# Kernel optimization log

Hardware: AMD Instinct MI355X
Metric: run time of the kernel (lower is better)

## Reference

```python
import jax, jax.numpy as jnp
import numpy as np

DIM = 256


def setup_inputs() -> dict:
    key = jax.random.key(0)
    ks = jax.random.split(key, 10)
    d = DIM
    inp = {
        "agent": jax.random.normal(ks[0], (64, d), dtype=jnp.float32),
        "x": jax.random.normal(ks[1], (8, 4096, d), dtype=jnp.float32),
        # parameters (stored as [in, out]; y = x @ W + b)
        "W_qkv": jax.random.normal(ks[2], (d, 3 * d), dtype=jnp.float32) * (d ** -0.5),
        "b_qkv": jnp.zeros((3 * d,), dtype=jnp.float32),
        "W_agent": jax.random.normal(ks[3], (d, 2 * d), dtype=jnp.float32) * (d ** -0.5),
        "b_agent": jnp.zeros((2 * d,), dtype=jnp.float32),
        "W_fc1": jax.random.normal(ks[4], (d, d), dtype=jnp.float32) * (d ** -0.5),
        "b_fc1": jnp.zeros((d,), dtype=jnp.float32),
        "W_fc2": jax.random.normal(ks[5], (d, d), dtype=jnp.float32) * (d ** -0.5),
        "b_fc2": jnp.zeros((d,), dtype=jnp.float32),
    }
    return inp


def reference(agent, x, W_qkv, b_qkv, W_agent, b_agent, W_fc1, b_fc1, W_fc2, b_fc2):
    d = x.shape[-1]
    scale = d ** -0.5
    # qkv projection of tokens: [B,N,3d] -> q,k,v each [B,N,d]
    qkv = x @ W_qkv + b_qkv
    q, k, v = jnp.split(qkv, 3, axis=-1)
    # agent projection: [K,2d] -> q_agent,k_agent each [K,d]
    ag = agent @ W_agent + b_agent
    q_agent, k_agent = jnp.split(ag, 2, axis=-1)
    # stage 1: agents attend over tokens -> [B,K,N]
    attn1 = jax.nn.softmax(jnp.einsum('kd,bnd->bkn', q_agent, k) * scale, axis=-1)
    va = jnp.einsum('bkn,bnd->bkd', attn1, v)  # [B,K,d]
    va = va @ W_fc1 + b_fc1
    # stage 2: tokens attend over agents -> [B,N,K]
    attn2 = jax.nn.softmax(jnp.einsum('bnd,kd->bnk', q, k_agent) * scale, axis=-1)
    out = jnp.einsum('bnk,bkd->bnd', attn2, va)  # [B,N,d]
    out = out @ W_fc2 + b_fc2
    return out + x
```

## Files before the change

kernel.cpp:

```cpp
#include <hip/hip_runtime.h>
#include <stdint.h>
#include <string.h>

#define BB 8
#define NN 4096
#define DD 256
#define SCALE 0.0625f
#define XS2 264

using frag_ab = __attribute__((ext_vector_type(8))) short;
using frag_cd = __attribute__((ext_vector_type(4))) float;

__device__ __forceinline__ unsigned short f2bf(float f) {
    union { float f; unsigned u; } a; a.f = f;
    unsigned r = a.u + 0x7FFFu + ((a.u >> 16) & 1u);
    return (unsigned short)(r >> 16);
}
__device__ __forceinline__ float bf2f(unsigned short h) {
    union { unsigned u; float f; } a; a.u = ((unsigned)h) << 16;
    return a.f;
}

__global__ __launch_bounds__(256) void k_setup(
    const float* __restrict__ agent, const float* __restrict__ Wag,
    const float* __restrict__ bag, const float* __restrict__ Wqkv,
    const float* __restrict__ bqkv, const float* __restrict__ Wfc1,
    const float* __restrict__ bfc1, const float* __restrict__ Wfc2,
    unsigned short* __restrict__ P12t, float* __restrict__ c2,
    unsigned short* __restrict__ W3b, float* __restrict__ b3)
{
    __shared__ float arow[256];
    __shared__ float red[256];
    const int bx = blockIdx.x, tid = threadIdx.x;
    if (bx < 128) {
        const int c = bx;
        const int woff = (c < 64) ? 256 : 0;
        const int aoff = (c < 64) ? 0 : 256;
        const int row = c & 63;
        float s = bag[aoff + tid];
        for (int o = 0; o < 256; ++o) s += agent[row * 256 + o] * Wag[o * 512 + aoff + tid];
        arow[tid] = s;
        __syncthreads();
        float p = 0.f;
        for (int o = 0; o < 256; ++o) p += Wqkv[tid * 768 + woff + o] * arow[o];
        P12t[(size_t)c * 256 + tid] = f2bf(SCALE * p);
        if (c >= 64) {
            red[tid] = bqkv[woff + tid] * arow[tid];
            __syncthreads();
            for (int st = 128; st; st >>= 1) {
                if (tid < st) red[tid] += red[tid + st];
                __syncthreads();
            }
            if (tid == 0) c2[c - 64] = SCALE * red[0];
        }
    } else if (bx < 384) {
        const int i = bx - 128;
        float t = 0.f;
        for (int o = 0; o < 256; ++o) t += Wqkv[i * 768 + 512 + o] * Wfc1[o * 256 + tid];
        arow[tid] = t;
        __syncthreads();
        float p = 0.f;
        for (int k = 0; k < 256; ++k) p += arow[k] * Wfc2[k * 256 + tid];
        W3b[(size_t)i * 256 + tid] = f2bf(p);
    } else {
        float t = bfc1[tid];
        for (int o = 0; o < 256; ++o) t += bqkv[512 + o] * Wfc1[o * 256 + tid];
        arow[tid] = t;
        __syncthreads();
        float p = 0.f;
        for (int k = 0; k < 256; ++k) p += arow[k] * Wfc2[k * 256 + tid];
        b3[tid] = p;
    }
}

__global__ __launch_bounds__(256) void k_xlogits(
    const float* __restrict__ x, const unsigned short* __restrict__ P12t,
    const float* __restrict__ c2, unsigned short* __restrict__ xt,
    unsigned short* __restrict__ p1, unsigned short* __restrict__ p2b,
    float* __restrict__ statS)
{
    __shared__ unsigned short xtile[32 * XS2];
    __shared__ unsigned short Bs[128 * 72];
    __shared__ float Ss[2][64];
    const int chunk = blockIdx.x, b = blockIdx.y;
    const int n0 = chunk * 32;
    const int tid = threadIdx.x;
    const int w = tid >> 6, lane = tid & 63;
    const int ml = lane & 15, q = lane >> 4;
    const int rt = w & 1, cg = w >> 1;

#pragma unroll
    for (int p = 0; p < 8; ++p) {
        int idx = p * 256 + tid;
        int tok = idx >> 6, d = (idx & 63) * 4;
        float4 v = *(const float4*)&x[(size_t)(b * 4096 + n0 + tok) * 256 + d];
        unsigned short u[4] = {f2bf(v.x), f2bf(v.y), f2bf(v.z), f2bf(v.w)};
        uint2 pk; memcpy(&pk, u, 8);
        *(uint2*)&xtile[tok * XS2 + d] = pk;
    }
    __syncthreads();
#pragma unroll
    for (int p = 0; p < 8; ++p) {
        int idx = p * 256 + tid;
        int d = idx >> 3, seg = idx & 7;
        unsigned short u[4];
#pragma unroll
        for (int k = 0; k < 4; ++k) u[k] = xtile[(seg * 4 + k) * XS2 + d];
        uint2 pk; memcpy(&pk, u, 8);
        *(uint2*)&xt[(size_t)(b * 256 + d) * 4096 + n0 + seg * 4] = pk;
    }

    frag_cd acc[4];
#pragma unroll
    for (int j = 0; j < 4; ++j)
#pragma unroll
        for (int r = 0; r < 4; ++r) acc[j][r] = 0.f;

    for (int kb = 0; kb < 256; kb += 64) {
        __syncthreads();
#pragma unroll
        for (int p = 0; p < 4; ++p) {
            int idx = p * 256 + tid;
            int r = idx >> 3, c = (idx & 7) * 8;
            *(uint4*)&Bs[r * 72 + c] = *(const uint4*)&P12t[(size_t)r * 256 + kb + c];
        }
        __syncthreads();
#pragma unroll
        for (int ks = 0; ks < 2; ++ks) {
            const int kk = ks * 32 + q * 8;
            frag_ab a = *(const frag_ab*)&xtile[(rt * 16 + ml) * XS2 + kb + kk];
#pragma unroll
            for (int j = 0; j < 4; ++j) {
                frag_ab bf = *(const frag_ab*)&Bs[(cg * 64 + j * 16 + ml) * 72 + kk];
                acc[j] = __builtin_amdgcn_mfma_f32_16x16x32_bf16(a, bf, acc[j], 0, 0, 0);
            }
        }
    }

    if (cg == 0) {
#pragma unroll
        for (int j = 0; j < 4; ++j) {
            const int ag = j * 16 + ml;
            float e[4];
#pragma unroll
            for (int r = 0; r < 4; ++r) e[r] = __expf(acc[j][r]);
            unsigned short u[4] = {f2bf(e[0]), f2bf(e[1]), f2bf(e[2]), f2bf(e[3])};
            uint2 pk; memcpy(&pk, u, 8);
            *(uint2*)&p1[(size_t)(b * 64 + ag) * 4096 + n0 + rt * 16 + q * 4] = pk;
            float s = e[0] + e[1] + e[2] + e[3];
            s += __shfl_xor(s, 16);
            s += __shfl_xor(s, 32);
            if (q == 0) Ss[rt][ag] = s;
        }
    } else {
        float cc[4];
#pragma unroll
        for (int j = 0; j < 4; ++j) cc[j] = c2[j * 16 + ml];
#pragma unroll
        for (int r = 0; r < 4; ++r) {
            float e[4], s = 0.f;
#pragma unroll
            for (int j = 0; j < 4; ++j) {
                e[j] = __expf(acc[j][r] + cc[j]);
                s += e[j];
            }
#pragma unroll
            for (int mask = 1; mask <= 8; mask <<= 1) s += __shfl_xor(s, mask);
            float inv = 1.f / s;
            const int tok = n0 + rt * 16 + q * 4 + r;
#pragma unroll
            for (int j = 0; j < 4; ++j)
                p2b[(size_t)(b * 4096 + tok) * 64 + j * 16 + ml] = f2bf(e[j] * inv);
        }
    }
    __syncthreads();
    if (tid < 64)
        statS[(size_t)(b * 64 + tid) * 128 + chunk] = Ss[0][tid] + Ss[1][tid];
}

__global__ __launch_bounds__(256) void k_va(
    const unsigned short* __restrict__ p1, const float* __restrict__ statS,
    const unsigned short* __restrict__ xt, unsigned short* __restrict__ part)
{
    __shared__ unsigned short As[64 * 152];
    __shared__ unsigned short Bs[64 * 152];
    __shared__ float Rs[4][64], Inv[64];
    const int s = blockIdx.x, dh = blockIdx.y, b = blockIdx.z;
    const int tid = threadIdx.x;
    const int w = tid >> 6, lane = tid & 63;
    const int ml = lane & 15, q = lane >> 4;

#pragma unroll
    for (int p = 0; p < 4; ++p) {
        int idx = p * 256 + tid;
        int r = idx >> 4, c = (idx & 15) * 8;
        *(uint4*)&Bs[r * 152 + c] =
            *(const uint4*)&xt[(size_t)(b * 256 + dh * 64 + r) * 4096 + s * 128 + c];
    }
    {
        const int a = tid & 63, qq = tid >> 6;
        const float* ps = &statS[(size_t)(b * 64 + a) * 128 + qq * 32];
        float sum = 0.f;
#pragma unroll
        for (int p = 0; p < 8; ++p) {
            float4 s4 = *(const float4*)&ps[p * 4];
            sum += s4.x + s4.y + s4.z + s4.w;
        }
        Rs[qq][a] = sum;
    }
    __syncthreads();
    if (tid < 64)
        Inv[tid] = 1.f / (Rs[0][tid] + Rs[1][tid] + Rs[2][tid] + Rs[3][tid]);
    __syncthreads();
#pragma unroll
    for (int p = 0; p < 8; ++p) {
        int idx4 = (p * 256 + tid) * 4;
        int ag = idx4 >> 7, t = idx4 & 127;
        uint2 pk = *(const uint2*)&p1[(size_t)(b * 64 + ag) * 4096 + s * 128 + t];
        unsigned short in[4]; memcpy(in, &pk, 8);
        float inv = Inv[ag];
        unsigned short u[4] = {f2bf(bf2f(in[0]) * inv), f2bf(bf2f(in[1]) * inv),
                               f2bf(bf2f(in[2]) * inv), f2bf(bf2f(in[3]) * inv)};
        uint2 po; memcpy(&po, u, 8);
        *(uint2*)&As[ag * 152 + t] = po;
    }
    __syncthreads();

    frag_cd acc[4];
#pragma unroll
    for (int i = 0; i < 4; ++i)
#pragma unroll
        for (int r = 0; r < 4; ++r) acc[i][r] = 0.f;
#pragma unroll
    for (int ks = 0; ks < 4; ++ks) {
        const int kk = ks * 32 + q * 8;
        frag_ab bf = *(const frag_ab*)&Bs[(w * 16 + ml) * 152 + kk];
#pragma unroll
        for (int i = 0; i < 4; ++i) {
            frag_ab a = *(const frag_ab*)&As[(i * 16 + ml) * 152 + kk];
            acc[i] = __builtin_amdgcn_mfma_f32_16x16x32_bf16(a, bf, acc[i], 0, 0, 0);
        }
    }
    const int d = dh * 64 + w * 16 + ml;
#pragma unroll
    for (int i = 0; i < 4; ++i)
#pragma unroll
        for (int r = 0; r < 4; ++r)
            part[(size_t)((s * 8 + b) * 64 + i * 16 + q * 4 + r) * 256 + d] =
                f2bf(acc[i][r]);
}

__global__ __launch_bounds__(256) void k_fc(
    const unsigned short* __restrict__ part, const unsigned short* __restrict__ W3b,
    const float* __restrict__ b3, unsigned short* __restrict__ va3t)
{
    __shared__ float rowb[256];
    const int row = blockIdx.x, tid = threadIdx.x;
    const int b = row >> 6, agc = row & 63;
    float sv = 0.f;
    for (int s = 0; s < 32; ++s)
        sv += bf2f(part[(size_t)((s * 8 + b) * 64 + agc) * 256 + tid]);
    rowb[tid] = sv;
    __syncthreads();
    float s2 = b3[tid];
    for (int k = 0; k < 256; ++k) s2 += rowb[k] * bf2f(W3b[(size_t)k * 256 + tid]);
    va3t[(size_t)(b * 256 + tid) * 64 + agc] = f2bf(s2);
}

__global__ __launch_bounds__(256) void k_stage2(
    const unsigned short* __restrict__ p2b, const unsigned short* __restrict__ va3t,
    const float* __restrict__ x, const float* __restrict__ bfc2,
    float* __restrict__ out)
{
    __shared__ unsigned short Vs[256 * 72];
    __shared__ unsigned short Ps[64 * 72];
    const int n0 = blockIdx.x * 64, b = blockIdx.y;
    const int tid = threadIdx.x;
    const int w = tid >> 6, lane = tid & 63;
    const int ml = lane & 15, q = lane >> 4;

#pragma unroll
    for (int p = 0; p < 8; ++p) {
        int idx = p * 256 + tid;
        int r = idx >> 3, c = (idx & 7) * 8;
        *(uint4*)&Vs[r * 72 + c] = *(const uint4*)&va3t[(size_t)(b * 256 + r) * 64 + c];
    }
#pragma unroll
    for (int p = 0; p < 2; ++p) {
        int idx = p * 256 + tid;
        int r = idx >> 3, c = (idx & 7) * 8;
        *(uint4*)&Ps[r * 72 + c] = *(const uint4*)&p2b[(size_t)(b * 4096 + n0 + r) * 64 + c];
    }
    __syncthreads();

    frag_cd acc[4][4];
#pragma unroll
    for (int i = 0; i < 4; ++i)
#pragma unroll
        for (int j = 0; j < 4; ++j)
#pragma unroll
            for (int r = 0; r < 4; ++r) acc[i][j][r] = 0.f;
#pragma unroll
    for (int ks = 0; ks < 2; ++ks) {
        const int kk = ks * 32 + q * 8;
        frag_ab a[4], bf[4];
#pragma unroll
        for (int i = 0; i < 4; ++i)
            a[i] = *(const frag_ab*)&Vs[(w * 64 + i * 16 + ml) * 72 + kk];
#pragma unroll
        for (int j = 0; j < 4; ++j)
            bf[j] = *(const frag_ab*)&Ps[(j * 16 + ml) * 72 + kk];
#pragma unroll
        for (int i = 0; i < 4; ++i)
#pragma unroll
            for (int j = 0; j < 4; ++j)
                acc[i][j] = __builtin_amdgcn_mfma_f32_16x16x32_bf16(
                    a[i], bf[j], acc[i][j], 0, 0, 0);
    }

#pragma unroll
    for (int i = 0; i < 4; ++i) {
        const int d0 = w * 64 + i * 16 + q * 4;
        float4 bias = *(const float4*)&bfc2[d0];
#pragma unroll
        for (int j = 0; j < 4; ++j) {
            const int tok = n0 + j * 16 + ml;
            size_t ad = (size_t)(b * 4096 + tok) * 256 + d0;
            float4 xr = *(const float4*)&x[ad];
            float4 o;
            o.x = acc[i][j][0] + bias.x + xr.x;
            o.y = acc[i][j][1] + bias.y + xr.y;
            o.z = acc[i][j][2] + bias.z + xr.z;
            o.w = acc[i][j][3] + bias.w + xr.w;
            *(float4*)&out[ad] = o;
        }
    }
}

extern "C" void kernel_launch(void* const* d_in, const int* in_sizes, int n_in,
                              void* d_out, int out_size, void* d_ws, size_t ws_size,
                              hipStream_t stream) {
    const float* agent = (const float*)d_in[0];
    const float* x     = (const float*)d_in[1];
    const float* Wqkv  = (const float*)d_in[2];
    const float* bqkv  = (const float*)d_in[3];
    const float* Wag   = (const float*)d_in[4];
    const float* bag   = (const float*)d_in[5];
    const float* Wfc1  = (const float*)d_in[6];
    const float* bfc1  = (const float*)d_in[7];
    const float* Wfc2  = (const float*)d_in[8];
    const float* bfc2  = (const float*)d_in[9];
    float* out = (float*)d_out;

    char* w = (char*)d_ws;
    size_t off = 0;
    unsigned short* xt   = (unsigned short*)(w + off); off += (size_t)BB * DD * NN * 2;
    unsigned short* p1   = (unsigned short*)(w + off); off += (size_t)BB * 64 * NN * 2;
    unsigned short* p2b  = (unsigned short*)(w + off); off += (size_t)BB * NN * 64 * 2;
    unsigned short* part = (unsigned short*)(w + off); off += (size_t)32 * BB * 64 * 256 * 2;
    float* statS = (float*)(w + off); off += (size_t)BB * 64 * 128 * 4;
    unsigned short* P12t = (unsigned short*)(w + off); off += (size_t)128 * 256 * 2;
    float* c2   = (float*)(w + off); off += 256 * 4;
    unsigned short* W3b = (unsigned short*)(w + off); off += (size_t)256 * 256 * 2;
    float* b3   = (float*)(w + off); off += 256 * 4;
    unsigned short* va3t = (unsigned short*)(w + off); off += (size_t)BB * DD * 64 * 2;

    k_setup<<<385, 256, 0, stream>>>(agent, Wag, bag, Wqkv, bqkv, Wfc1, bfc1, Wfc2,
                                     P12t, c2, W3b, b3);
    k_xlogits<<<dim3(128, BB), 256, 0, stream>>>(x, P12t, c2, xt, p1, p2b, statS);
    k_va<<<dim3(32, 4, BB), 256, 0, stream>>>(p1, statS, xt, part);
    k_fc<<<512, 256, 0, stream>>>(part, W3b, b3, va3t);
    k_stage2<<<dim3(64, BB), 256, 0, stream>>>(p2b, va3t, x, bfc2, out);
}
```

Baseline: 169.0 us.

## Load MFMA operands directly from global memory and shrink stage2 tiles

Several kernels stop staging operands in shared memory. k_xlogits reads the P12t fragments and k_va reads the xt fragments straight from global memory, which drops their LDS buffers and barriers. k_stage2 halves its token tile to 32, doubles its grid, prefetches the residual x early and loads fragments directly from global. k_setup vectorises its dot product with float4, and k_va widens its p1 loads to 16 bytes. Direct global fragment loads depend on L2 and L1 hits and may produce less coalesced accesses.

```diff
diff --git a/kernel.cpp b/kernel.cpp
--- a/kernel.cpp
+++ b/kernel.cpp
@@ -42,7 +42,13 @@
         arow[tid] = s;
         __syncthreads();
         float p = 0.f;
-        for (int o = 0; o < 256; ++o) p += Wqkv[tid * 768 + woff + o] * arow[o];
+        const float* wr = &Wqkv[tid * 768 + woff];
+#pragma unroll 8
+        for (int o4 = 0; o4 < 64; ++o4) {
+            float4 wv = *(const float4*)&wr[o4 * 4];
+            float4 av = *(const float4*)&arow[o4 * 4];
+            p += wv.x * av.x + wv.y * av.y + wv.z * av.z + wv.w * av.w;
+        }
         P12t[(size_t)c * 256 + tid] = f2bf(SCALE * p);
         if (c >= 64) {
             red[tid] = bqkv[woff + tid] * arow[tid];
@@ -80,7 +86,6 @@
     float* __restrict__ statS)
 {
     __shared__ unsigned short xtile[32 * XS2];
-    __shared__ unsigned short Bs[128 * 72];
     __shared__ float Ss[2][64];
     const int chunk = blockIdx.x, b = blockIdx.y;
     const int n0 = chunk * 32;
@@ -116,22 +121,15 @@
 #pragma unroll
         for (int r = 0; r < 4; ++r) acc[j][r] = 0.f;
 
-    for (int kb = 0; kb < 256; kb += 64) {
-        __syncthreads();
-#pragma unroll
-        for (int p = 0; p < 4; ++p) {
-            int idx = p * 256 + tid;
-            int r = idx >> 3, c = (idx & 7) * 8;
-            *(uint4*)&Bs[r * 72 + c] = *(const uint4*)&P12t[(size_t)r * 256 + kb + c];
-        }
-        __syncthreads();
+#pragma unroll
+    for (int kb = 0; kb < 4; ++kb) {
 #pragma unroll
         for (int ks = 0; ks < 2; ++ks) {
-            const int kk = ks * 32 + q * 8;
-            frag_ab a = *(const frag_ab*)&xtile[(rt * 16 + ml) * XS2 + kb + kk];
+            const int kk = kb * 64 + ks * 32 + q * 8;
+            frag_ab a = *(const frag_ab*)&xtile[(rt * 16 + ml) * XS2 + kk];
 #pragma unroll
             for (int j = 0; j < 4; ++j) {
-                frag_ab bf = *(const frag_ab*)&Bs[(cg * 64 + j * 16 + ml) * 72 + kk];
+                frag_ab bf = *(const frag_ab*)&P12t[(size_t)(cg * 64 + j * 16 + ml) * 256 + kk];
                 acc[j] = __builtin_amdgcn_mfma_f32_16x16x32_bf16(a, bf, acc[j], 0, 0, 0);
             }
         }
@@ -183,20 +181,12 @@
     const unsigned short* __restrict__ xt, unsigned short* __restrict__ part)
 {
     __shared__ unsigned short As[64 * 152];
-    __shared__ unsigned short Bs[64 * 152];
     __shared__ float Rs[4][64], Inv[64];
     const int s = blockIdx.x, dh = blockIdx.y, b = blockIdx.z;
     const int tid = threadIdx.x;
     const int w = tid >> 6, lane = tid & 63;
     const int ml = lane & 15, q = lane >> 4;
 
-#pragma unroll
-    for (int p = 0; p < 4; ++p) {
-        int idx = p * 256 + tid;
-        int r = idx >> 4, c = (idx & 15) * 8;
-        *(uint4*)&Bs[r * 152 + c] =
-            *(const uint4*)&xt[(size_t)(b * 256 + dh * 64 + r) * 4096 + s * 128 + c];
-    }
     {
         const int a = tid & 63, qq = tid >> 6;
         const float* ps = &statS[(size_t)(b * 64 + a) * 128 + qq * 32];
@@ -213,16 +203,17 @@
         Inv[tid] = 1.f / (Rs[0][tid] + Rs[1][tid] + Rs[2][tid] + Rs[3][tid]);
     __syncthreads();
 #pragma unroll
-    for (int p = 0; p < 8; ++p) {
-        int idx4 = (p * 256 + tid) * 4;
-        int ag = idx4 >> 7, t = idx4 & 127;
-        uint2 pk = *(const uint2*)&p1[(size_t)(b * 64 + ag) * 4096 + s * 128 + t];
-        unsigned short in[4]; memcpy(in, &pk, 8);
+    for (int p = 0; p < 4; ++p) {
+        int idx8 = (p * 256 + tid) * 8;
+        int ag = idx8 >> 7, t = idx8 & 127;
+        uint4 pk = *(const uint4*)&p1[(size_t)(b * 64 + ag) * 4096 + s * 128 + t];
+        unsigned short in[8]; memcpy(in, &pk, 16);
         float inv = Inv[ag];
-        unsigned short u[4] = {f2bf(bf2f(in[0]) * inv), f2bf(bf2f(in[1]) * inv),
-                               f2bf(bf2f(in[2]) * inv), f2bf(bf2f(in[3]) * inv)};
-        uint2 po; memcpy(&po, u, 8);
-        *(uint2*)&As[ag * 152 + t] = po;
+        unsigned short u[8];
+#pragma unroll
+        for (int k = 0; k < 8; ++k) u[k] = f2bf(bf2f(in[k]) * inv);
+        uint4 po; memcpy(&po, u, 16);
+        *(uint4*)&As[ag * 152 + t] = po;
     }
     __syncthreads();
 
@@ -234,7 +225,8 @@
 #pragma unroll
     for (int ks = 0; ks < 4; ++ks) {
         const int kk = ks * 32 + q * 8;
-        frag_ab bf = *(const frag_ab*)&Bs[(w * 16 + ml) * 152 + kk];
+        frag_ab bf = *(const frag_ab*)&xt[(size_t)(b * 256 + dh * 64 + w * 16 + ml) * 4096 +
+                                          s * 128 + kk];
 #pragma unroll
         for (int i = 0; i < 4; ++i) {
             frag_ab a = *(const frag_ab*)&As[(i * 16 + ml) * 152 + kk];
@@ -272,66 +264,59 @@
     const float* __restrict__ x, const float* __restrict__ bfc2,
     float* __restrict__ out)
 {
-    __shared__ unsigned short Vs[256 * 72];
-    __shared__ unsigned short Ps[64 * 72];
-    const int n0 = blockIdx.x * 64, b = blockIdx.y;
+    const int n0 = blockIdx.x * 32, b = blockIdx.y;
     const int tid = threadIdx.x;
     const int w = tid >> 6, lane = tid & 63;
     const int ml = lane & 15, q = lane >> 4;
 
-#pragma unroll
-    for (int p = 0; p < 8; ++p) {
-        int idx = p * 256 + tid;
-        int r = idx >> 3, c = (idx & 7) * 8;
-        *(uint4*)&Vs[r * 72 + c] = *(const uint4*)&va3t[(size_t)(b * 256 + r) * 64 + c];
-    }
-#pragma unroll
-    for (int p = 0; p < 2; ++p) {
-        int idx = p * 256 + tid;
-        int r = idx >> 3, c = (idx & 7) * 8;
-        *(uint4*)&Ps[r * 72 + c] = *(const uint4*)&p2b[(size_t)(b * 4096 + n0 + r) * 64 + c];
-    }
-    __syncthreads();
-
-    frag_cd acc[4][4];
+    float4 xr[4][2];
 #pragma unroll
     for (int i = 0; i < 4; ++i)
 #pragma unroll
-        for (int j = 0; j < 4; ++j)
-#pragma unroll
-            for (int r = 0; r < 4; ++r) acc[i][j][r] = 0.f;
+        for (int j = 0; j < 2; ++j)
+            xr[i][j] = *(const float4*)&x[(size_t)(b * 4096 + n0 + j * 16 + ml) * 256 +
+                                          w * 64 + i * 16 + q * 4];
+
+    frag_ab a[4][2], bf[2][2];
 #pragma unroll
     for (int ks = 0; ks < 2; ++ks) {
         const int kk = ks * 32 + q * 8;
-        frag_ab a[4], bf[4];
 #pragma unroll
         for (int i = 0; i < 4; ++i)
-            a[i] = *(const frag_ab*)&Vs[(w * 64 + i * 16 + ml) * 72 + kk];
-#pragma unroll
-        for (int j = 0; j < 4; ++j)
-            bf[j] = *(const frag_ab*)&Ps[(j * 16 + ml) * 72 + kk];
+            a[i][ks] = *(const frag_ab*)&va3t[(size_t)(b * 256 + w * 64 + i * 16 + ml) * 64 + kk];
+#pragma unroll
+        for (int j = 0; j < 2; ++j)
+            bf[j][ks] = *(const frag_ab*)&p2b[(size_t)(b * 4096 + n0 + j * 16 + ml) * 64 + kk];
+    }
+
+    frag_cd acc[4][2];
+#pragma unroll
+    for (int i = 0; i < 4; ++i)
+#pragma unroll
+        for (int j = 0; j < 2; ++j)
+#pragma unroll
+            for (int r = 0; r < 4; ++r) acc[i][j][r] = 0.f;
+#pragma unroll
+    for (int ks = 0; ks < 2; ++ks)
 #pragma unroll
         for (int i = 0; i < 4; ++i)
 #pragma unroll
-            for (int j = 0; j < 4; ++j)
+            for (int j = 0; j < 2; ++j)
                 acc[i][j] = __builtin_amdgcn_mfma_f32_16x16x32_bf16(
-                    a[i], bf[j], acc[i][j], 0, 0, 0);
-    }
+                    a[i][ks], bf[j][ks], acc[i][j], 0, 0, 0);
 
 #pragma unroll
     for (int i = 0; i < 4; ++i) {
         const int d0 = w * 64 + i * 16 + q * 4;
         float4 bias = *(const float4*)&bfc2[d0];
 #pragma unroll
-        for (int j = 0; j < 4; ++j) {
-            const int tok = n0 + j * 16 + ml;
-            size_t ad = (size_t)(b * 4096 + tok) * 256 + d0;
-            float4 xr = *(const float4*)&x[ad];
+        for (int j = 0; j < 2; ++j) {
+            size_t ad = (size_t)(b * 4096 + n0 + j * 16 + ml) * 256 + d0;
             float4 o;
-            o.x = acc[i][j][0] + bias.x + xr.x;
-            o.y = acc[i][j][1] + bias.y + xr.y;
-            o.z = acc[i][j][2] + bias.z + xr.z;
-            o.w = acc[i][j][3] + bias.w + xr.w;
+            o.x = acc[i][j][0] + bias.x + xr[i][j].x;
+            o.y = acc[i][j][1] + bias.y + xr[i][j].y;
+            o.z = acc[i][j][2] + bias.z + xr[i][j].z;
+            o.w = acc[i][j][3] + bias.w + xr[i][j].w;
             *(float4*)&out[ad] = o;
         }
     }
@@ -370,5 +355,5 @@
     k_xlogits<<<dim3(128, BB), 256, 0, stream>>>(x, P12t, c2, xt, p1, p2b, statS);
     k_va<<<dim3(32, 4, BB), 256, 0, stream>>>(p1, statS, xt, part);
     k_fc<<<512, 256, 0, stream>>>(part, W3b, b3, va3t);
-    k_stage2<<<dim3(64, BB), 256, 0, stream>>>(p2b, va3t, x, bfc2, out);
-}
+    k_stage2<<<dim3(128, BB), 256, 0, stream>>>(p2b, va3t, x, bfc2, out);
+}
```

New measurement: 180.7 us. +6.9%, slower.
